# Kernel tuning notes

Measured on AMD Instinct MI355X. Metric: run time of the kernel, lower is better.

The kernel has to match this reference:

```python
import jax, jax.numpy as jnp
import numpy as np

T, K = 3, 3  # filter_size = [T, K, K]
PAD = K // 2


def setup_inputs() -> dict:
    key = jax.random.key(0)
    k1, k2 = jax.random.split(key)
    B, H, W, C_out = 8, 192, 192, 16
    x = jax.random.normal(k1, (B, T, H, W), dtype=jnp.float32)
    f = jax.random.normal(k2, (B, H, W, T * K * K, C_out), dtype=jnp.float32)
    return {"x": x, "f": f}


def _im2col(x):
    # x: (B, T, H, W) -> patches (B, H, W, K*K*T), channel order (kh, kw, t)
    # matching eye(27).reshape(K, K, T, 27) used as a TF HWIO conv filter
    # with SAME padding.
    B, Tt, H, W = x.shape
    xp = jnp.pad(x, ((0, 0), (0, 0), (PAD, PAD), (PAD, PAD)))
    cols = [xp[:, t, i:i + H, j:j + W]
            for i in range(K) for j in range(K) for t in range(Tt)]
    return jnp.stack(cols, axis=-1)  # (B, H, W, K*K*T)


def reference(x, f):
    # per-pixel dynamic filtering: out[b,h,w,o] = sum_k patches[b,h,w,k] * f[b,h,w,k,o]
    patches = _im2col(x)  # (B, H, W, 27)
    return jnp.einsum('bhwk,bhwko->bhwo', patches, f)  # (B, H, W, C_out)
```

## Files before the change

kernel.cpp:

```cpp
#include <hip/hip_runtime.h>


#define B_ 8
#define T_ 3
#define H_ 192
#define W_ 192
#define CO_ 16
#define KT_ 27
#define PIX_PER_BLK 64
#define XS_N (3 * 3 * 66)

__global__ __launch_bounds__(256) void DynFilter3D_kernel(
    const float* __restrict__ x,
    const float* __restrict__ f,
    float* __restrict__ out)
{
    int blk = blockIdx.x;
    int wt  = blk % 3;
    int bh  = blk / 3;
    int h   = bh % H_;
    int b   = bh / H_;
    int w0  = wt * PIX_PER_BLK;

    __shared__ float xs[XS_N];

    for (int idx = threadIdx.x; idx < XS_N; idx += 256) {
        int wwp = idx % 66;
        int ti  = idx / 66;
        int i   = ti % 3;
        int t   = ti / 3;
        int hh  = h + i - 1;
        int ww  = w0 + wwp - 1;
        float v = 0.0f;
        if ((unsigned)hh < (unsigned)H_ && (unsigned)ww < (unsigned)W_)
            v = x[(size_t)((b * T_ + t) * H_ + hh) * W_ + ww];
        xs[idx] = v;
    }
    __syncthreads();

    int wl = threadIdx.x >> 2;
    int t4 = threadIdx.x & 3;

    float patches[KT_];
#pragma unroll
    for (int i = 0; i < 3; ++i)
#pragma unroll
        for (int j = 0; j < 3; ++j)
#pragma unroll
            for (int t = 0; t < 3; ++t)
                patches[(i * 3 + j) * 3 + t] = xs[(t * 3 + i) * 66 + wl + j];

    size_t pix = (size_t)(b * H_ + h) * W_ + w0 + wl;
    const float4* fb = reinterpret_cast<const float4*>(f + pix * (KT_ * CO_));
    float4 acc = make_float4(0.f, 0.f, 0.f, 0.f);
#pragma unroll
    for (int k = 0; k < KT_; ++k) {
        float4 fv = fb[k * 4 + t4];
        float  p  = patches[k];
        acc.x = fmaf(p, fv.x, acc.x);
        acc.y = fmaf(p, fv.y, acc.y);
        acc.z = fmaf(p, fv.z, acc.z);
        acc.w = fmaf(p, fv.w, acc.w);
    }

    reinterpret_cast<float4*>(out + pix * CO_)[t4] = acc;
}

extern "C" void kernel_launch(void* const* d_in, const int* in_sizes, int n_in,
                              void* d_out, int out_size, void* d_ws, size_t ws_size,
                              hipStream_t stream) {
    const float* x = (const float*)d_in[0];
    const float* f = (const float*)d_in[1];
    float* out = (float*)d_out;

    const int grid = B_ * H_ * 3;
    DynFilter3D_kernel<<<grid, 256, 0, stream>>>(x, f, out);
}
```

Measured before the change: 98.75 us.

## Split each pixel's filter reduction across 8 threads with shared patch staging

Halves pixels per block and assigns 8 threads per pixel, so consecutive lanes read contiguous float4 chunks of the per-pixel filter and the large filter stream coalesces better. Patches are staged into a shared-memory array indexed by pixel and tap, and the two partial sums per output are combined with a lane shuffle. This adds an extra shared-memory pass, a barrier and a shuffle reduction, and doubles the number of blocks.

```diff
diff --git a/kernel.cpp b/kernel.cpp
--- a/kernel.cpp
+++ b/kernel.cpp
@@ -7,8 +7,10 @@
 #define W_ 192
 #define CO_ 16
 #define KT_ 27
-#define PIX_PER_BLK 64
-#define XS_N (3 * 3 * 66)
+#define PIX_PER_BLK 32
+#define HALO_W 34
+#define XS_N (3 * 3 * HALO_W)
+#define PL_N (PIX_PER_BLK * KT_)
 
 __global__ __launch_bounds__(256) void DynFilter3D_kernel(
     const float* __restrict__ x,
@@ -16,21 +18,22 @@
     float* __restrict__ out)
 {
     int blk = blockIdx.x;
-    int wt  = blk % 3;
-    int bh  = blk / 3;
+    int wt  = blk % 6;
+    int bh  = blk / 6;
     int h   = bh % H_;
     int b   = bh / H_;
     int w0  = wt * PIX_PER_BLK;
 
     __shared__ float xs[XS_N];
+    __shared__ float pl[PL_N];
 
     for (int idx = threadIdx.x; idx < XS_N; idx += 256) {
-        int wwp = idx % 66;
-        int ti  = idx / 66;
-        int i   = ti % 3;
-        int t   = ti / 3;
-        int hh  = h + i - 1;
-        int ww  = w0 + wwp - 1;
+        int wp = idx % HALO_W;
+        int ti = idx / HALO_W;
+        int i  = ti % 3;
+        int t  = ti / 3;
+        int hh = h + i - 1;
+        int ww = w0 + wp - 1;
         float v = 0.0f;
         if ((unsigned)hh < (unsigned)H_ && (unsigned)ww < (unsigned)W_)
             v = x[(size_t)((b * T_ + t) * H_ + hh) * W_ + ww];
@@ -38,32 +41,46 @@
     }
     __syncthreads();
 
-    int wl = threadIdx.x >> 2;
-    int t4 = threadIdx.x & 3;
+    for (int idx = threadIdx.x; idx < PL_N; idx += 256) {
+        int k  = idx % KT_;
+        int pxl = idx / KT_;
+        int t  = k % 3;
+        int ij = k / 3;
+        int jw = ij % 3;
+        int i  = ij / 3;
+        pl[idx] = xs[(t * 3 + i) * HALO_W + pxl + jw];
+    }
+    __syncthreads();
 
-    float patches[KT_];
-#pragma unroll
-    for (int i = 0; i < 3; ++i)
-#pragma unroll
-        for (int j = 0; j < 3; ++j)
-#pragma unroll
-            for (int t = 0; t < 3; ++t)
-                patches[(i * 3 + j) * 3 + t] = xs[(t * 3 + i) * 66 + wl + j];
+    int wl = threadIdx.x >> 3;
+    int j  = threadIdx.x & 7;
+    int k0 = j >> 2;
+    size_t pix = (size_t)(b * H_ + h) * W_ + w0 + wl;
 
-    size_t pix = (size_t)(b * H_ + h) * W_ + w0 + wl;
     const float4* fb = reinterpret_cast<const float4*>(f + pix * (KT_ * CO_));
+    const float*  pp = pl + wl * KT_ + k0;
+
     float4 acc = make_float4(0.f, 0.f, 0.f, 0.f);
 #pragma unroll
-    for (int k = 0; k < KT_; ++k) {
-        float4 fv = fb[k * 4 + t4];
-        float  p  = patches[k];
-        acc.x = fmaf(p, fv.x, acc.x);
-        acc.y = fmaf(p, fv.y, acc.y);
-        acc.z = fmaf(p, fv.z, acc.z);
-        acc.w = fmaf(p, fv.w, acc.w);
+    for (int m = 0; m < 14; ++m) {
+        int e = j + 8 * m;
+        if (e < KT_ * 4) {
+            float4 fv = fb[e];
+            float  p  = pp[2 * m];
+            acc.x = fmaf(p, fv.x, acc.x);
+            acc.y = fmaf(p, fv.y, acc.y);
+            acc.z = fmaf(p, fv.z, acc.z);
+            acc.w = fmaf(p, fv.w, acc.w);
+        }
     }
 
-    reinterpret_cast<float4*>(out + pix * CO_)[t4] = acc;
+    acc.x += __shfl_xor(acc.x, 4);
+    acc.y += __shfl_xor(acc.y, 4);
+    acc.z += __shfl_xor(acc.z, 4);
+    acc.w += __shfl_xor(acc.w, 4);
+
+    if (j < 4)
+        reinterpret_cast<float4*>(out + pix * CO_)[j] = acc;
 }
 
 extern "C" void kernel_launch(void* const* d_in, const int* in_sizes, int n_in,
@@ -73,6 +90,6 @@
     const float* f = (const float*)d_in[1];
     float* out = (float*)d_out;
 
-    const int grid = B_ * H_ * 3;
+    const int grid = B_ * H_ * (W_ / PIX_PER_BLK);
     DynFilter3D_kernel<<<grid, 256, 0, stream>>>(x, f, out);
 }
```

After: 97.19 us (median of 2 runs). No clear change (-1.6%).
